# Performance work log

Hardware: AMD Instinct MI355X
Metric: run time of the kernel (lower is better)

The kernel has to match this reference:

```python
import jax, jax.numpy as jnp
import numpy as np
import math

B, T, DIM, H = 2, 2048, 1024, 16
HD = DIM // H


def setup_inputs() -> dict:
    key = jax.random.key(0)
    ks = jax.random.split(key, 5)
    s = 1.0 / math.sqrt(DIM)
    return {
        "x": jax.random.normal(ks[0], (B, T, DIM), dtype=jnp.float32),
        "wq": jax.random.normal(ks[1], (DIM, DIM), dtype=jnp.float32) * s,
        "wk": jax.random.normal(ks[2], (DIM, DIM), dtype=jnp.float32) * s,
        "wv": jax.random.normal(ks[3], (DIM, DIM), dtype=jnp.float32) * s,
        "wo": jax.random.normal(ks[4], (DIM, DIM), dtype=jnp.float32) * s,
    }


def reference(x, wq, wk, wv, wo):
    Bc, Tc, C = x.shape
    # nn.Linear applies x @ W.T; weights here stored as [out, in]
    def proj(w):
        return (x @ w.T).reshape(Bc, Tc, H, HD).transpose(0, 2, 1, 3)  # [B,H,T,hd]
    q, k, v = proj(wq), proj(wk), proj(wv)
    scores = jnp.einsum("bhqd,bhkd->bhqk", q, k) / math.sqrt(HD)
    causal = jnp.tril(jnp.ones((Tc, Tc), dtype=bool))
    scores = jnp.where(causal, scores, -jnp.inf)
    attn = jax.nn.softmax(scores, axis=-1)
    out = jnp.einsum("bhqk,bhkd->bhqd", attn, v)
    out = out.transpose(0, 2, 1, 3).reshape(Bc, Tc, C)
    return out @ wo.T
```

## Files before the change

### kernel.cpp

```cpp
#include <hip/hip_runtime.h>
#include <stdint.h>


#define T_SEQ 2048
#define QSCALE 0.1803368801111204f

typedef unsigned short u16;
typedef __attribute__((ext_vector_type(8))) __bf16 bf16x8;
typedef __attribute__((ext_vector_type(4))) float  f32x4;

#define NEG_BIG (-30000.0f)

__device__ __forceinline__ u16 f2bf(float x) {
    union { float f; unsigned u; } c; c.f = x;
    return (u16)((c.u + 0x7fffu + ((c.u >> 16) & 1u)) >> 16);
}

__device__ __forceinline__ void gload_lds16(const void* g, void* l) {
    __builtin_amdgcn_global_load_lds(
        (const __attribute__((address_space(1))) void*)g,
        (__attribute__((address_space(3))) void*)l, 16, 0, 0);
}

__device__ __forceinline__ void storeC(u16* p, float v)   { *p = f2bf(v); }
__device__ __forceinline__ void storeC(float* p, float v) { *p = v; }

__global__ __launch_bounds__(256) void cvt_all(
    const float* __restrict__ x,  const float* __restrict__ wq,
    const float* __restrict__ wk, const float* __restrict__ wv,
    const float* __restrict__ wo, u16* __restrict__ xb, u16* __restrict__ wb)
{
    int i = blockIdx.x * 256 + threadIdx.x;
    const float* s; u16* d; int off;
    if (i < 1048576) { s = x; d = xb; off = i; }
    else {
        int j = i - 1048576;
        int wsel = j >> 18;
        off = j & 262143;
        s = wsel == 0 ? wq : wsel == 1 ? wk : wsel == 2 ? wv : wo;
        d = wb + (size_t)wsel * 1048576u;
    }
    float4 v = ((const float4*)s)[off];
    ushort4 o;
    o.x = f2bf(v.x); o.y = f2bf(v.y); o.z = f2bf(v.z); o.w = f2bf(v.w);
    ((ushort4*)d)[off] = o;
}

template <typename OutT, bool VT_MODE>
__global__ __launch_bounds__(256) void gemm_bt(
    const u16* __restrict__ A, const u16* __restrict__ Wb,
    OutT* __restrict__ C0, OutT* __restrict__ C1, OutT* __restrict__ C2)
{
    __shared__ __align__(16) char As[128 * 128];
    __shared__ __align__(16) char Bs[128 * 128];

    const u16* W = Wb + (size_t)blockIdx.z * 1048576u;
    OutT* Cz = blockIdx.z == 0 ? C0 : (blockIdx.z == 1 ? C1 : C2);

    const int tid = threadIdx.x;
    const int w = tid >> 6, l = tid & 63;
    const int wy = w >> 1, wx = w & 1;
    const int bm = blockIdx.y * 128, bn = blockIdx.x * 128;

    f32x4 acc[4][4];
#pragma unroll
    for (int m = 0; m < 4; m++)
#pragma unroll
        for (int n = 0; n < 4; n++) acc[m][n] = (f32x4){0.f, 0.f, 0.f, 0.f};

    const int lrow = l >> 3, lslot = l & 7;

    for (int kt = 0; kt < 16; ++kt) {
#pragma unroll
        for (int c = 0; c < 4; ++c) {
            int ch = w * 4 + c;
            int row = ch * 8 + lrow;
            gload_lds16((const char*)A + ((size_t)(bm + row) * 1024 + kt * 64) * 2 + lslot * 16,
                        As + ch * 1024);
            gload_lds16((const char*)W + ((size_t)(bn + row) * 1024 + kt * 64) * 2 + lslot * 16,
                        Bs + ch * 1024);
        }
        __syncthreads();

#pragma unroll
        for (int kk = 0; kk < 2; ++kk) {
            const int cb = (kk * 32 + (l >> 4) * 8) * 2;
            bf16x8 af[4], bfr[4];
#pragma unroll
            for (int m = 0; m < 4; m++)
                af[m] = *(const bf16x8*)(As + (wy * 64 + m * 16 + (l & 15)) * 128 + cb);
#pragma unroll
            for (int n = 0; n < 4; n++)
                bfr[n] = *(const bf16x8*)(Bs + (wx * 64 + n * 16 + (l & 15)) * 128 + cb);
#pragma unroll
            for (int m = 0; m < 4; m++)
#pragma unroll
                for (int n = 0; n < 4; n++)
                    acc[m][n] = __builtin_amdgcn_mfma_f32_16x16x32_bf16(
                        af[m], bfr[n], acc[m][n], 0, 0, 0);
        }
        __syncthreads();
    }

    const bool vtw = VT_MODE && (blockIdx.z == 2);
    const float osc = (VT_MODE && blockIdx.z == 0) ? QSCALE : 1.0f;
#pragma unroll
    for (int m = 0; m < 4; m++) {
        int grow0 = bm + wy * 64 + m * 16 + (l >> 4) * 4;
#pragma unroll
        for (int n = 0; n < 4; n++) {
            int gcol = bn + wx * 64 + n * 16 + (l & 15);
            if (vtw) {
                int bh = (grow0 >> 11) * 16 + (gcol >> 6);
                size_t rowbase = ((size_t)bh * 64 + (gcol & 63)) * T_SEQ + (grow0 & 2047);
#pragma unroll
                for (int r = 0; r < 4; r++)
                    storeC(&Cz[rowbase + r], acc[m][n][r]);
            } else {
#pragma unroll
                for (int r = 0; r < 4; r++)
                    storeC(&Cz[(size_t)(grow0 + r) * 1024 + gcol], acc[m][n][r] * osc);
            }
        }
    }
}

__device__ __forceinline__ void online_sm(
    f32x4 (&s)[4], f32x4 (&oacc)[4], float& mrun, float& lrun,
    int qrow_g, int kbase, bool diag, int g, u16 (*__restrict__ Ps)[72], int q16)
{
    if (diag) {
#pragma unroll
        for (int nt = 0; nt < 4; ++nt)
#pragma unroll
            for (int r = 0; r < 4; ++r)
                if (kbase + nt * 16 + g * 4 + r > qrow_g) s[nt][r] = NEG_BIG;
    }
    float a0 = fmaxf(fmaxf(s[0][0], s[0][1]), fmaxf(s[0][2], s[0][3]));
    float a1 = fmaxf(fmaxf(s[1][0], s[1][1]), fmaxf(s[1][2], s[1][3]));
    float a2 = fmaxf(fmaxf(s[2][0], s[2][1]), fmaxf(s[2][2], s[2][3]));
    float a3 = fmaxf(fmaxf(s[3][0], s[3][1]), fmaxf(s[3][2], s[3][3]));
    float pm = fmaxf(fmaxf(a0, a1), fmaxf(a2, a3));
    pm = fmaxf(pm, __shfl_xor(pm, 16));
    pm = fmaxf(pm, __shfl_xor(pm, 32));

    const bool noresc = __all(pm <= mrun + 8.0f);
    const float mnew = noresc ? mrun : fmaxf(mrun, pm);

#pragma unroll
    for (int nt = 0; nt < 4; ++nt)
#pragma unroll
        for (int r = 0; r < 4; ++r)
            s[nt][r] = __builtin_amdgcn_exp2f(s[nt][r] - mnew);

    float b0 = (s[0][0] + s[0][1]) + (s[0][2] + s[0][3]);
    float b1 = (s[1][0] + s[1][1]) + (s[1][2] + s[1][3]);
    float b2 = (s[2][0] + s[2][1]) + (s[2][2] + s[2][3]);
    float b3 = (s[3][0] + s[3][1]) + (s[3][2] + s[3][3]);
    float rs = (b0 + b1) + (b2 + b3);
    rs += __shfl_xor(rs, 16);
    rs += __shfl_xor(rs, 32);

    if (!noresc) {
        float alpha = __builtin_amdgcn_exp2f(mrun - mnew);
        lrun *= alpha;
#pragma unroll
        for (int nt = 0; nt < 4; ++nt)
#pragma unroll
            for (int r = 0; r < 4; ++r) oacc[nt][r] *= alpha;
        mrun = mnew;
    }
    lrun += rs;

#pragma unroll
    for (int nt = 0; nt < 4; ++nt) {
        ushort4 pk;
        pk.x = f2bf(s[nt][0]); pk.y = f2bf(s[nt][1]);
        pk.z = f2bf(s[nt][2]); pk.w = f2bf(s[nt][3]);
        *(ushort4*)(&Ps[q16][nt * 16 + g * 4]) = pk;
    }
}

__global__ __launch_bounds__(64) void attn_fwd(
    const u16* __restrict__ Q, const u16* __restrict__ K,
    const u16* __restrict__ VT, u16* __restrict__ O)
{
    __shared__ __align__(16) u16 PsA[16][72];
    __shared__ __align__(16) u16 PsB[16][72];

    const int bh = blockIdx.x;
    const int y0 = blockIdx.y;
    const int y = (y0 & 1) ? (63 - (y0 >> 1)) : (y0 >> 1);
    const int b = bh >> 4, h = bh & 15;
    const int l = threadIdx.x;
    const int g = l >> 4, q16 = l & 15;
    const size_t base = (size_t)b * T_SEQ * 1024 + h * 64;
    const u16* vtb = VT + (size_t)bh * 64 * T_SEQ;

    const int qgA = y * 32, qgB = qgA + 16;
    const int qrA = qgA + q16, qrB = qgB + q16;
    const int ktmax = (qgA + 31) >> 6;

    const u16* qpA = Q + base + (size_t)qrA * 1024 + g * 8;
    const u16* qpB = Q + base + (size_t)qrB * 1024 + g * 8;
    bf16x8 qfA[2], qfB[2];
    qfA[0] = *(const bf16x8*)(qpA); qfA[1] = *(const bf16x8*)(qpA + 32);
    qfB[0] = *(const bf16x8*)(qpB); qfB[1] = *(const bf16x8*)(qpB + 32);

    f32x4 oaccA[4], oaccB[4];
#pragma unroll
    for (int n = 0; n < 4; n++) {
        oaccA[n] = (f32x4){0.f, 0.f, 0.f, 0.f};
        oaccB[n] = (f32x4){0.f, 0.f, 0.f, 0.f};
    }
    float mA = NEG_BIG, lA = 0.f, mB = NEG_BIG, lB = 0.f;

    auto run_iter = [&](int kt, bool diag) {
        const int kbase = kt * 64;

        bf16x8 kf[2][4], vf[2][4];
#pragma unroll
        for (int kk = 0; kk < 2; ++kk)
#pragma unroll
            for (int nt = 0; nt < 4; ++nt) {
                kf[kk][nt] = *(const bf16x8*)(K + base
                    + (size_t)(kbase + nt * 16 + q16) * 1024 + kk * 32 + g * 8);
                vf[kk][nt] = *(const bf16x8*)(vtb
                    + (size_t)(nt * 16 + q16) * T_SEQ + kbase + kk * 32 + g * 8);
            }

        f32x4 sA[4], sB[4];
#pragma unroll
        for (int n = 0; n < 4; n++) {
            sA[n] = (f32x4){0.f, 0.f, 0.f, 0.f};
            sB[n] = (f32x4){0.f, 0.f, 0.f, 0.f};
        }
#pragma unroll
        for (int kk = 0; kk < 2; ++kk)
#pragma unroll
            for (int nt = 0; nt < 4; ++nt) {
                if (!diag || (kbase + nt * 16 <= qgA + 15))
                    sA[nt] = __builtin_amdgcn_mfma_f32_16x16x32_bf16(
                        kf[kk][nt], qfA[kk], sA[nt], 0, 0, 0);
                if (!diag || (kbase + nt * 16 <= qgB + 15))
                    sB[nt] = __builtin_amdgcn_mfma_f32_16x16x32_bf16(
                        kf[kk][nt], qfB[kk], sB[nt], 0, 0, 0);
            }

        online_sm(sA, oaccA, mA, lA, qrA, kbase, diag, g, PsA, q16);
        online_sm(sB, oaccB, mB, lB, qrB, kbase, diag, g, PsB, q16);

#pragma unroll
        for (int kk = 0; kk < 2; ++kk) {
            bf16x8 pfA = *(const bf16x8*)(&PsA[q16][kk * 32 + g * 8]);
            bf16x8 pfB = *(const bf16x8*)(&PsB[q16][kk * 32 + g * 8]);
            const bool okA = !diag || (kbase + kk * 32 <= qgA + 15);
            const bool okB = !diag || (kbase + kk * 32 <= qgB + 15);
#pragma unroll
            for (int nt = 0; nt < 4; ++nt) {
                if (okA)
                    oaccA[nt] = __builtin_amdgcn_mfma_f32_16x16x32_bf16(
                        vf[kk][nt], pfA, oaccA[nt], 0, 0, 0);
                if (okB)
                    oaccB[nt] = __builtin_amdgcn_mfma_f32_16x16x32_bf16(
                        vf[kk][nt], pfB, oaccB[nt], 0, 0, 0);
            }
        }
    };

    for (int kt = 0; kt < ktmax; ++kt) run_iter(kt, false);
    run_iter(ktmax, true);

    const float riA = __builtin_amdgcn_rcpf(lA);
    const float riB = __builtin_amdgcn_rcpf(lB);
    u16* orowA = O + (size_t)b * T_SEQ * 1024 + (size_t)qrA * 1024 + h * 64;
    u16* orowB = O + (size_t)b * T_SEQ * 1024 + (size_t)qrB * 1024 + h * 64;
#pragma unroll
    for (int nt = 0; nt < 4; ++nt) {
        ushort4 oa, ob;
        oa.x = f2bf(oaccA[nt][0] * riA); oa.y = f2bf(oaccA[nt][1] * riA);
        oa.z = f2bf(oaccA[nt][2] * riA); oa.w = f2bf(oaccA[nt][3] * riA);
        ob.x = f2bf(oaccB[nt][0] * riB); ob.y = f2bf(oaccB[nt][1] * riB);
        ob.z = f2bf(oaccB[nt][2] * riB); ob.w = f2bf(oaccB[nt][3] * riB);
        *(ushort4*)(orowA + nt * 16 + g * 4) = oa;
        *(ushort4*)(orowB + nt * 16 + g * 4) = ob;
    }
}

extern "C" void kernel_launch(void* const* d_in, const int* in_sizes, int n_in,
                              void* d_out, int out_size, void* d_ws, size_t ws_size,
                              hipStream_t stream)
{
    (void)in_sizes; (void)n_in; (void)out_size; (void)ws_size;
    const float* x  = (const float*)d_in[0];
    const float* wq = (const float*)d_in[1];
    const float* wk = (const float*)d_in[2];
    const float* wv = (const float*)d_in[3];
    const float* wo = (const float*)d_in[4];
    float* out = (float*)d_out;

    char* ws = (char*)d_ws;
    u16* xb = (u16*)(ws);
    u16* wb = (u16*)(ws + (8u << 20));
    u16* Kb = (u16*)(ws + (16u << 20));
    u16* VT = (u16*)(ws + (24u << 20));
    u16* Ob = (u16*)(ws + (32u << 20));
    u16* Qb = (u16*)d_out;

    dim3 blk(256);
    cvt_all<<<8192, blk, 0, stream>>>(x, wq, wk, wv, wo, xb, wb);

    gemm_bt<u16, true><<<dim3(8, 32, 3), blk, 0, stream>>>(xb, wb, Qb, Kb, VT);
    attn_fwd<<<dim3(32, 64, 1), dim3(64), 0, stream>>>(Qb, Kb, VT, Ob);
    gemm_bt<float, false><<<dim3(8, 32, 1), blk, 0, stream>>>(Ob, wb + 3u * 1048576u,
                                                              out, out, out);
}
```

Baseline: 257.9 us.

## Pair query tile j with tile 127-j per block to balance causal work

Each block now handles two 16-row query tiles taken from opposite ends of the sequence (j and 127-j) instead of two adjacent tiles. Every block therefore does roughly the same number of key tiles, which should remove load imbalance from the causal triangle. K/V fragments are shared between the two tiles only up to tile j's diagonal. After that a B-only loop loads K/V for one tile, so total fragment traffic per useful MFMA goes up.

```diff
diff --git a/kernel.cpp b/kernel.cpp
--- a/kernel.cpp
+++ b/kernel.cpp
@@ -189,17 +189,16 @@
     __shared__ __align__(16) u16 PsB[16][72];
 
     const int bh = blockIdx.x;
-    const int y0 = blockIdx.y;
-    const int y = (y0 & 1) ? (63 - (y0 >> 1)) : (y0 >> 1);
+    const int j = blockIdx.y;
     const int b = bh >> 4, h = bh & 15;
     const int l = threadIdx.x;
     const int g = l >> 4, q16 = l & 15;
     const size_t base = (size_t)b * T_SEQ * 1024 + h * 64;
     const u16* vtb = VT + (size_t)bh * 64 * T_SEQ;
 
-    const int qgA = y * 32, qgB = qgA + 16;
+    const int qgA = j * 16, qgB = (127 - j) * 16;
     const int qrA = qgA + q16, qrB = qgB + q16;
-    const int ktmax = (qgA + 31) >> 6;
+    const int ktmaxA = j >> 2, ktmaxB = (127 - j) >> 2;
 
     const u16* qpA = Q + base + (size_t)qrA * 1024 + g * 8;
     const u16* qpB = Q + base + (size_t)qrB * 1024 + g * 8;
@@ -215,10 +214,8 @@
     }
     float mA = NEG_BIG, lA = 0.f, mB = NEG_BIG, lB = 0.f;
 
-    auto run_iter = [&](int kt, bool diag) {
-        const int kbase = kt * 64;
-
-        bf16x8 kf[2][4], vf[2][4];
+    bf16x8 kf[2][4], vf[2][4];
+    auto load_frags = [&](int kbase) {
 #pragma unroll
         for (int kk = 0; kk < 2; ++kk)
 #pragma unroll
@@ -228,6 +225,11 @@
                 vf[kk][nt] = *(const bf16x8*)(vtb
                     + (size_t)(nt * 16 + q16) * T_SEQ + kbase + kk * 32 + g * 8);
             }
+    };
+
+    auto iter_both = [&](int kt, bool diagA) {
+        const int kbase = kt * 64;
+        load_frags(kbase);
 
         f32x4 sA[4], sB[4];
 #pragma unroll
@@ -239,28 +241,56 @@
         for (int kk = 0; kk < 2; ++kk)
 #pragma unroll
             for (int nt = 0; nt < 4; ++nt) {
-                if (!diag || (kbase + nt * 16 <= qgA + 15))
+                if (!diagA || (kbase + nt * 16 <= qgA + 15))
                     sA[nt] = __builtin_amdgcn_mfma_f32_16x16x32_bf16(
                         kf[kk][nt], qfA[kk], sA[nt], 0, 0, 0);
-                if (!diag || (kbase + nt * 16 <= qgB + 15))
-                    sB[nt] = __builtin_amdgcn_mfma_f32_16x16x32_bf16(
-                        kf[kk][nt], qfB[kk], sB[nt], 0, 0, 0);
-            }
-
-        online_sm(sA, oaccA, mA, lA, qrA, kbase, diag, g, PsA, q16);
-        online_sm(sB, oaccB, mB, lB, qrB, kbase, diag, g, PsB, q16);
+                sB[nt] = __builtin_amdgcn_mfma_f32_16x16x32_bf16(
+                    kf[kk][nt], qfB[kk], sB[nt], 0, 0, 0);
+            }
+
+        online_sm(sA, oaccA, mA, lA, qrA, kbase, diagA, g, PsA, q16);
+        online_sm(sB, oaccB, mB, lB, qrB, kbase, false, g, PsB, q16);
 
 #pragma unroll
         for (int kk = 0; kk < 2; ++kk) {
             bf16x8 pfA = *(const bf16x8*)(&PsA[q16][kk * 32 + g * 8]);
             bf16x8 pfB = *(const bf16x8*)(&PsB[q16][kk * 32 + g * 8]);
-            const bool okA = !diag || (kbase + kk * 32 <= qgA + 15);
-            const bool okB = !diag || (kbase + kk * 32 <= qgB + 15);
+            const bool okA = !diagA || (kbase + kk * 32 <= qgA + 15);
 #pragma unroll
             for (int nt = 0; nt < 4; ++nt) {
                 if (okA)
                     oaccA[nt] = __builtin_amdgcn_mfma_f32_16x16x32_bf16(
                         vf[kk][nt], pfA, oaccA[nt], 0, 0, 0);
+                oaccB[nt] = __builtin_amdgcn_mfma_f32_16x16x32_bf16(
+                    vf[kk][nt], pfB, oaccB[nt], 0, 0, 0);
+            }
+        }
+    };
+
+    auto iter_B = [&](int kt, bool diagB) {
+        const int kbase = kt * 64;
+        load_frags(kbase);
+
+        f32x4 sB[4];
+#pragma unroll
+        for (int n = 0; n < 4; n++) sB[n] = (f32x4){0.f, 0.f, 0.f, 0.f};
+#pragma unroll
+        for (int kk = 0; kk < 2; ++kk)
+#pragma unroll
+            for (int nt = 0; nt < 4; ++nt) {
+                if (!diagB || (kbase + nt * 16 <= qgB + 15))
+                    sB[nt] = __builtin_amdgcn_mfma_f32_16x16x32_bf16(
+                        kf[kk][nt], qfB[kk], sB[nt], 0, 0, 0);
+            }
+
+        online_sm(sB, oaccB, mB, lB, qrB, kbase, diagB, g, PsB, q16);
+
+#pragma unroll
+        for (int kk = 0; kk < 2; ++kk) {
+            bf16x8 pfB = *(const bf16x8*)(&PsB[q16][kk * 32 + g * 8]);
+            const bool okB = !diagB || (kbase + kk * 32 <= qgB + 15);
+#pragma unroll
+            for (int nt = 0; nt < 4; ++nt) {
                 if (okB)
                     oaccB[nt] = __builtin_amdgcn_mfma_f32_16x16x32_bf16(
                         vf[kk][nt], pfB, oaccB[nt], 0, 0, 0);
@@ -268,8 +298,10 @@
         }
     };
 
-    for (int kt = 0; kt < ktmax; ++kt) run_iter(kt, false);
-    run_iter(ktmax, true);
+    for (int kt = 0; kt < ktmaxA; ++kt) iter_both(kt, false);
+    iter_both(ktmaxA, true);
+    for (int kt = ktmaxA + 1; kt < ktmaxB; ++kt) iter_B(kt, false);
+    iter_B(ktmaxB, true);
 
     const float riA = __builtin_amdgcn_rcpf(lA);
     const float riB = __builtin_amdgcn_rcpf(lB);
```

Result: no change. 257.7 us (-0.1%).

## Pair mirrored query tiles per block and double-buffer K/V register loads

Applied to the files above, without the earlier changes.

Each block now handles query tile j and its mirror 127-j, so every block does the same amount of causal work. Before, the two 16-row tiles were adjacent and load balance came from interleaving the blockIdx.y order. K/V fragments for the next 64-key tile are loaded into a second register set while the current tile is computed, to hide global-load latency. Tile A's MFMAs and softmax are skipped once it passes its diagonal. Launch bounds now request one block per CU, which raises register pressure and can lower occupancy.

```diff
diff --git a/kernel.cpp b/kernel.cpp
--- a/kernel.cpp
+++ b/kernel.cpp
@@ -181,7 +181,7 @@
     }
 }
 
-__global__ __launch_bounds__(64) void attn_fwd(
+__global__ __launch_bounds__(64, 1) void attn_fwd(
     const u16* __restrict__ Q, const u16* __restrict__ K,
     const u16* __restrict__ VT, u16* __restrict__ O)
 {
@@ -189,17 +189,16 @@
     __shared__ __align__(16) u16 PsB[16][72];
 
     const int bh = blockIdx.x;
-    const int y0 = blockIdx.y;
-    const int y = (y0 & 1) ? (63 - (y0 >> 1)) : (y0 >> 1);
+    const int j = blockIdx.y;
     const int b = bh >> 4, h = bh & 15;
     const int l = threadIdx.x;
     const int g = l >> 4, q16 = l & 15;
     const size_t base = (size_t)b * T_SEQ * 1024 + h * 64;
     const u16* vtb = VT + (size_t)bh * 64 * T_SEQ;
 
-    const int qgA = y * 32, qgB = qgA + 16;
+    const int qgA = j * 16, qgB = (127 - j) * 16;
     const int qrA = qgA + q16, qrB = qgB + q16;
-    const int ktmax = (qgA + 31) >> 6;
+    const int ktA = j >> 2, ktB = (127 - j) >> 2;
 
     const u16* qpA = Q + base + (size_t)qrA * 1024 + g * 8;
     const u16* qpB = Q + base + (size_t)qrB * 1024 + g * 8;
@@ -215,10 +214,9 @@
     }
     float mA = NEG_BIG, lA = 0.f, mB = NEG_BIG, lB = 0.f;
 
-    auto run_iter = [&](int kt, bool diag) {
-        const int kbase = kt * 64;
-
-        bf16x8 kf[2][4], vf[2][4];
+    bf16x8 kfa[2][4], vfa[2][4], kfb[2][4], vfb[2][4];
+
+    auto lf = [&](int kbase, bf16x8 (&kf)[2][4], bf16x8 (&vf)[2][4]) {
 #pragma unroll
         for (int kk = 0; kk < 2; ++kk)
 #pragma unroll
@@ -228,6 +226,12 @@
                 vf[kk][nt] = *(const bf16x8*)(vtb
                     + (size_t)(nt * 16 + q16) * T_SEQ + kbase + kk * 32 + g * 8);
             }
+    };
+
+    auto body = [&](int t, bf16x8 (&kf)[2][4], bf16x8 (&vf)[2][4]) {
+        const int kbase = t * 64;
+        const bool actA = (t <= ktA);
+        const bool dA = (t == ktA), dB = (t == ktB);
 
         f32x4 sA[4], sB[4];
 #pragma unroll
@@ -235,41 +239,55 @@
             sA[n] = (f32x4){0.f, 0.f, 0.f, 0.f};
             sB[n] = (f32x4){0.f, 0.f, 0.f, 0.f};
         }
-#pragma unroll
-        for (int kk = 0; kk < 2; ++kk)
-#pragma unroll
-            for (int nt = 0; nt < 4; ++nt) {
-                if (!diag || (kbase + nt * 16 <= qgA + 15))
+        if (actA) {
+#pragma unroll
+            for (int kk = 0; kk < 2; ++kk)
+#pragma unroll
+                for (int nt = 0; nt < 4; ++nt)
                     sA[nt] = __builtin_amdgcn_mfma_f32_16x16x32_bf16(
                         kf[kk][nt], qfA[kk], sA[nt], 0, 0, 0);
-                if (!diag || (kbase + nt * 16 <= qgB + 15))
-                    sB[nt] = __builtin_amdgcn_mfma_f32_16x16x32_bf16(
-                        kf[kk][nt], qfB[kk], sB[nt], 0, 0, 0);
-            }
-
-        online_sm(sA, oaccA, mA, lA, qrA, kbase, diag, g, PsA, q16);
-        online_sm(sB, oaccB, mB, lB, qrB, kbase, diag, g, PsB, q16);
+        }
+#pragma unroll
+        for (int kk = 0; kk < 2; ++kk)
+#pragma unroll
+            for (int nt = 0; nt < 4; ++nt)
+                sB[nt] = __builtin_amdgcn_mfma_f32_16x16x32_bf16(
+                    kf[kk][nt], qfB[kk], sB[nt], 0, 0, 0);
+
+        if (actA) online_sm(sA, oaccA, mA, lA, qrA, kbase, dA, g, PsA, q16);
+        online_sm(sB, oaccB, mB, lB, qrB, kbase, dB, g, PsB, q16);
 
 #pragma unroll
         for (int kk = 0; kk < 2; ++kk) {
-            bf16x8 pfA = *(const bf16x8*)(&PsA[q16][kk * 32 + g * 8]);
             bf16x8 pfB = *(const bf16x8*)(&PsB[q16][kk * 32 + g * 8]);
-            const bool okA = !diag || (kbase + kk * 32 <= qgA + 15);
-            const bool okB = !diag || (kbase + kk * 32 <= qgB + 15);
-#pragma unroll
-            for (int nt = 0; nt < 4; ++nt) {
-                if (okA)
+#pragma unroll
+            for (int nt = 0; nt < 4; ++nt)
+                oaccB[nt] = __builtin_amdgcn_mfma_f32_16x16x32_bf16(
+                    vf[kk][nt], pfB, oaccB[nt], 0, 0, 0);
+        }
+        if (actA) {
+#pragma unroll
+            for (int kk = 0; kk < 2; ++kk) {
+                bf16x8 pfA = *(const bf16x8*)(&PsA[q16][kk * 32 + g * 8]);
+#pragma unroll
+                for (int nt = 0; nt < 4; ++nt)
                     oaccA[nt] = __builtin_amdgcn_mfma_f32_16x16x32_bf16(
                         vf[kk][nt], pfA, oaccA[nt], 0, 0, 0);
-                if (okB)
-                    oaccB[nt] = __builtin_amdgcn_mfma_f32_16x16x32_bf16(
-                        vf[kk][nt], pfB, oaccB[nt], 0, 0, 0);
             }
         }
     };
 
-    for (int kt = 0; kt < ktmax; ++kt) run_iter(kt, false);
-    run_iter(ktmax, true);
+    lf(0, kfa, vfa);
+    const int npair = (ktB + 2) >> 1;
+    for (int p = 0; p < npair; ++p) {
+        const int t0 = 2 * p, t1 = 2 * p + 1;
+        if (t0 < ktB) lf((t0 + 1) * 64, kfb, vfb);
+        body(t0, kfa, vfa);
+        if (t1 <= ktB) {
+            if (t1 < ktB) lf((t1 + 1) * 64, kfa, vfa);
+            body(t1, kfb, vfb);
+        }
+    }
 
     const float riA = __builtin_amdgcn_rcpf(lA);
     const float riB = __builtin_amdgcn_rcpf(lB);
```

Result: no change. 255.2 us (-1.0%).
